# Performance work log

Measured on AMD Instinct MI355X. Metric: run time of the kernel, lower is better.

## Reference

```python
import jax, jax.numpy as jnp
import numpy as np

NREF, NALT, B, D, F = 131072, 32768, 4096, 128, 512
H = F // 2  # d_ffn // 2
EPS = 1e-5


def _ln(x, w, b):
    m = jnp.mean(x, axis=-1, keepdims=True)
    v = jnp.mean((x - m) ** 2, axis=-1, keepdims=True)
    return (x - m) * jax.lax.rsqrt(v + EPS) * w + b


def setup_inputs() -> dict:
    key = jax.random.key(0)
    ks = jax.random.split(key, 16)
    s = 0.02
    return {
        "ref_flat": jax.random.normal(ks[0], (NREF, D), jnp.float32),
        "alt_flat": jax.random.normal(ks[1], (NALT, D), jnp.float32),
        "ref_seg": jnp.sort(jax.random.randint(ks[2], (NREF,), 0, B)),
        "alt_seg": jnp.sort(jax.random.randint(ks[3], (NALT,), 0, B)),
        "norm1_w": jnp.ones((D,), jnp.float32),
        "norm1_b": jnp.zeros((D,), jnp.float32),
        "w1_ref": jax.random.normal(ks[4], (D, F), jnp.float32) * s,
        "b1_ref": jnp.zeros((F,), jnp.float32),
        "w1_alt": jax.random.normal(ks[5], (D, F), jnp.float32) * s,
        "b1_alt": jnp.zeros((F,), jnp.float32),
        "norm2_w": jnp.ones((H,), jnp.float32),
        "norm2_b": jnp.zeros((H,), jnp.float32),
        "alpha_ref": jnp.float32(0.01),
        "alpha_alt": jnp.float32(0.01),
        "beta_ref": jnp.float32(0.01),
        "beta_alt": jnp.float32(0.01),
        "gamma": jnp.float32(0.01),
        "ref_regularizer": 0.1 * jnp.ones((H,), jnp.float32),
        "reg_w_pre": jnp.float32(np.log(0.1)),
        "w2_ref": jax.random.normal(ks[6], (H, D), jnp.float32) * s,
        "b2_ref": jnp.zeros((D,), jnp.float32),
        "w2_alt": jax.random.normal(ks[7], (H, D), jnp.float32) * s,
        "b2_alt": jnp.zeros((D,), jnp.float32),
    }


def reference(ref_flat, alt_flat, ref_seg, alt_seg,
              norm1_w, norm1_b, w1_ref, b1_ref, w1_alt, b1_alt,
              norm2_w, norm2_b, alpha_ref, alpha_alt, beta_ref, beta_alt,
              gamma, ref_regularizer, reg_w_pre, w2_ref, b2_ref, w2_alt, b2_alt):
    # proj1 + SELU on flattened ragged reads
    zr = jax.nn.selu(_ln(ref_flat, norm1_w, norm1_b) @ w1_ref + b1_ref)   # [NREF, F]
    za = jax.nn.selu(_ln(alt_flat, norm1_w, norm1_b) @ w1_alt + b1_alt)   # [NALT, F]
    z1r, z2r = zr[:, :H], zr[:, H:]
    z1a, z2a = za[:, :H], za[:, H:]
    z2r = _ln(z2r, norm2_w, norm2_b)
    z2a = _ln(z2a, norm2_w, norm2_b)

    cnt_r = jax.ops.segment_sum(jnp.ones((NREF,), z2r.dtype), ref_seg, num_segments=B)
    cnt_a = jax.ops.segment_sum(jnp.ones((NALT,), z2a.dtype), alt_seg, num_segments=B)
    reg_w = jnp.exp(reg_w_pre) + 0.25
    # regularized mean field over each ref set
    ref_mf = (jax.ops.segment_sum(z2r, ref_seg, num_segments=B)
              + reg_w * ref_regularizer) / (cnt_r[:, None] + reg_w)       # [B, H]
    alt_mf = jax.ops.segment_sum(z2a, alt_seg, num_segments=B) \
             / jnp.maximum(cnt_a, 1.0)[:, None]                            # [B, H]

    ref_gate = z2r * alpha_ref + 1.0 + (beta_ref * ref_mf)[ref_seg]
    alt_gate = z2a * alpha_alt + 1.0 + (beta_alt * alt_mf + gamma * ref_mf)[alt_seg]

    out_r = ref_flat + (z1r * ref_gate) @ w2_ref + b2_ref
    out_a = alt_flat + (z1a * alt_gate) @ w2_alt + b2_alt
    return out_r, out_a
```

## Files before the change

### kernel.cpp

```cpp
#include <hip/hip_runtime.h>
#include <hip/hip_bf16.h>

#define NREF 131072
#define NALT 32768
#define BSEG 4096
#define D 128
#define F 512
#define H 256
#define EPS 1e-5f

typedef short short8 __attribute__((ext_vector_type(8)));
typedef float f32x4 __attribute__((ext_vector_type(4)));

__device__ __forceinline__ float selu_f(float z) {
    const float sc = 1.0507009873554805f;
    const float al = 1.6732632423543772f;
    return z > 0.f ? sc * z : sc * al * (__expf(z) - 1.f);
}

__device__ __forceinline__ short f2bf(float v) {
    __bf16 b = (__bf16)v;
    return __builtin_bit_cast(short, b);
}

__global__ void pack_w(const float* __restrict__ w, __bf16* __restrict__ wp, int KT, int N) {
    int idx = blockIdx.x * 256 + threadIdx.x;
    int j = idx & 7;
    int l = (idx >> 3) & 63;
    int t = idx >> 9;
    int kt = t % KT;
    int nt = t / KT;
    int k = kt * 32 + ((l >> 4) << 3) + j;
    int n = (nt << 4) + (l & 15);
    wp[idx] = (__bf16)w[k * N + n];
}

__global__ __launch_bounds__(256, 3)
void pass1_kernel(const float* __restrict__ x, const int* __restrict__ seg,
                  const __bf16* __restrict__ w1p, const float* __restrict__ b1,
                  const float* __restrict__ n1w, const float* __restrict__ n1b,
                  const float* __restrict__ n2w, const float* __restrict__ n2b,
                  float* __restrict__ seg_sum, float* __restrict__ seg_cnt) {
    __shared__ __align__(16) __bf16 ys[32 * 128];
    __shared__ float z2s[32][257];
    __shared__ float n2w_s[H], n2b_s[H], b1h_s[H];
    __shared__ int seg_s[32];

    const int tid = threadIdx.x;
    const int lane = tid & 63;
    const int wv = tid >> 6;
    const size_t row0 = (size_t)blockIdx.x * 32;

    short8 bb[4][4];
    #pragma unroll
    for (int p = 0; p < 4; ++p)
        #pragma unroll
        for (int kt = 0; kt < 4; ++kt)
            bb[p][kt] = *reinterpret_cast<const short8*>(
                w1p + ((size_t)((16 + wv * 4 + p) * 4 + kt) * 64 + lane) * 8);

    const int r = tid >> 3, g = tid & 7;
    float xr[16];
    #pragma unroll
    for (int i = 0; i < 4; ++i) {
        float4 t = *reinterpret_cast<const float4*>(x + (row0 + r) * D + g * 16 + i * 4);
        xr[i * 4 + 0] = t.x; xr[i * 4 + 1] = t.y; xr[i * 4 + 2] = t.z; xr[i * 4 + 3] = t.w;
    }
    float w1r[16], c1r[16];
    #pragma unroll
    for (int i = 0; i < 4; ++i) {
        float4 t = *reinterpret_cast<const float4*>(n1w + g * 16 + i * 4);
        w1r[i * 4 + 0] = t.x; w1r[i * 4 + 1] = t.y; w1r[i * 4 + 2] = t.z; w1r[i * 4 + 3] = t.w;
        float4 u = *reinterpret_cast<const float4*>(n1b + g * 16 + i * 4);
        c1r[i * 4 + 0] = u.x; c1r[i * 4 + 1] = u.y; c1r[i * 4 + 2] = u.z; c1r[i * 4 + 3] = u.w;
    }

    n2w_s[tid] = n2w[tid]; n2b_s[tid] = n2b[tid];
    b1h_s[tid] = b1[H + tid];
    if (tid < 32) seg_s[tid] = seg[row0 + tid];

    {
        float s = 0.f, ss = 0.f;
        #pragma unroll
        for (int i = 0; i < 16; ++i) { s += xr[i]; ss += xr[i] * xr[i]; }
        s += __shfl_xor(s, 1); ss += __shfl_xor(ss, 1);
        s += __shfl_xor(s, 2); ss += __shfl_xor(ss, 2);
        s += __shfl_xor(s, 4); ss += __shfl_xor(ss, 4);
        float mean = s * (1.f / 128.f);
        float var = ss * (1.f / 128.f) - mean * mean;
        float rsv = rsqrtf(var + EPS);
        const int swr = (r & 7) << 3;
        #pragma unroll
        for (int h = 0; h < 2; ++h) {
            short8 pk;
            #pragma unroll
            for (int j = 0; j < 8; ++j) {
                pk[j] = f2bf((xr[h * 8 + j] - mean) * rsv * w1r[h * 8 + j] + c1r[h * 8 + j]);
            }
            *reinterpret_cast<short8*>(&ys[r * 128 + ((g * 16 + h * 8) ^ swr)]) = pk;
        }
    }
    __syncthreads();

    {
        const int m0 = lane & 15;
        const int swm = (m0 & 7) << 3;
        const int ccol = (lane >> 4) << 3;
        short8 a0[4], a1[4];
        #pragma unroll
        for (int kt = 0; kt < 4; ++kt) {
            a0[kt] = *reinterpret_cast<const short8*>(&ys[m0 * 128 + ((kt * 32 + ccol) ^ swm)]);
            a1[kt] = *reinterpret_cast<const short8*>(&ys[(m0 + 16) * 128 + ((kt * 32 + ccol) ^ swm)]);
        }
        #pragma unroll
        for (int nt = 0; nt < 4; ++nt) {
            f32x4 acc0 = {0.f, 0.f, 0.f, 0.f};
            f32x4 acc1 = {0.f, 0.f, 0.f, 0.f};
            #pragma unroll
            for (int kt = 0; kt < 4; ++kt) {
                acc0 = __builtin_amdgcn_mfma_f32_16x16x32_bf16(a0[kt], bb[nt][kt], acc0, 0, 0, 0);
                acc1 = __builtin_amdgcn_mfma_f32_16x16x32_bf16(a1[kt], bb[nt][kt], acc1, 0, 0, 0);
            }
            int cz = (wv * 4 + nt) * 16 + m0;
            float bbias = b1h_s[cz];
            #pragma unroll
            for (int reg = 0; reg < 4; ++reg) {
                int r0 = ((lane >> 4) << 2) + reg;
                z2s[r0][cz] = selu_f(acc0[reg] + bbias);
                z2s[r0 + 16][cz] = selu_f(acc1[reg] + bbias);
            }
        }
    }
    __syncthreads();

    {
        float s2 = 0.f, q2 = 0.f;
        float z2c[32];
        #pragma unroll
        for (int c = 0; c < 32; ++c) {
            int col = g * 4 + (c & 3) + ((c >> 2) << 5);
            float v = z2s[r][col];
            z2c[c] = v; s2 += v; q2 += v * v;
        }
        s2 += __shfl_xor(s2, 1); q2 += __shfl_xor(q2, 1);
        s2 += __shfl_xor(s2, 2); q2 += __shfl_xor(q2, 2);
        s2 += __shfl_xor(s2, 4); q2 += __shfl_xor(q2, 4);
        float mean2 = s2 * (1.f / 256.f);
        float var2 = q2 * (1.f / 256.f) - mean2 * mean2;
        float rs2 = rsqrtf(var2 + EPS);
        #pragma unroll
        for (int c = 0; c < 32; ++c) {
            int col = g * 4 + (c & 3) + ((c >> 2) << 5);
            z2s[r][col] = (z2c[c] - mean2) * rs2 * n2w_s[col] + n2b_s[col];
        }
    }
    __syncthreads();

    {
        int c = tid;
        int s_cur = seg_s[0];
        float run = 0.f;
        for (int rr = 0; rr < 32; ++rr) {
            int sg = seg_s[rr];
            if (sg != s_cur) {
                atomicAdd(&seg_sum[(size_t)s_cur * H + c], run);
                run = 0.f; s_cur = sg;
            }
            run += z2s[rr][c];
        }
        atomicAdd(&seg_sum[(size_t)s_cur * H + c], run);
        if (tid == 0) {
            int sc = seg_s[0]; float rl = 0.f;
            for (int rr = 0; rr < 32; ++rr) {
                if (seg_s[rr] != sc) { atomicAdd(&seg_cnt[sc], rl); rl = 0.f; sc = seg_s[rr]; }
                rl += 1.f;
            }
            atomicAdd(&seg_cnt[sc], rl);
        }
    }
}

__global__ void mf_kernel(const float* __restrict__ sum_r, const float* __restrict__ cnt_r,
                          const float* __restrict__ sum_a, const float* __restrict__ cnt_a,
                          const float* __restrict__ regz, const float* __restrict__ reg_w_pre,
                          const float* __restrict__ beta_ref, const float* __restrict__ beta_alt,
                          const float* __restrict__ gamma,
                          float* __restrict__ G_ref, float* __restrict__ G_alt) {
    int s = blockIdx.x, c = threadIdx.x;
    size_t i = (size_t)s * H + c;
    float rw = __expf(reg_w_pre[0]) + 0.25f;
    float mfr = (sum_r[i] + rw * regz[c]) / (cnt_r[s] + rw);
    float mfa = sum_a[i] / fmaxf(cnt_a[s], 1.f);
    G_ref[i] = beta_ref[0] * mfr;
    G_alt[i] = beta_alt[0] * mfa + gamma[0] * mfr;
}

__global__ __launch_bounds__(256, 3)
void pass2_kernel(const float* __restrict__ x, const int* __restrict__ seg,
                  const __bf16* __restrict__ w1p, const float* __restrict__ b1,
                  const __bf16* __restrict__ w2p, const float* __restrict__ b2,
                  const float* __restrict__ n1w, const float* __restrict__ n1b,
                  const float* __restrict__ n2w, const float* __restrict__ n2b,
                  const float* __restrict__ alpha_p, const float* __restrict__ G,
                  float* __restrict__ out) {
    __shared__ __align__(16) __bf16 ys[32 * 128];
    __shared__ __align__(16) __bf16 zs[32 * 512];
    __shared__ float n2w_s[H], n2b_s[H], b1_s[F], b2_s[D];
    __shared__ int seg_s[32];
    __shared__ float alpha_s;

    const int tid = threadIdx.x;
    const int lane = tid & 63;
    const int wv = tid >> 6;
    const size_t row0 = (size_t)blockIdx.x * 32;

    short8 bb[4][4];
    #pragma unroll
    for (int p = 0; p < 4; ++p)
        #pragma unroll
        for (int kt = 0; kt < 4; ++kt)
            bb[p][kt] = *reinterpret_cast<const short8*>(
                w1p + ((size_t)((wv * 8 + p) * 4 + kt) * 64 + lane) * 8);

    const int r = tid >> 3, g = tid & 7;
    float xr[16];
    #pragma unroll
    for (int i = 0; i < 4; ++i) {
        float4 t = *reinterpret_cast<const float4*>(x + (row0 + r) * D + g * 16 + i * 4);
        xr[i * 4 + 0] = t.x; xr[i * 4 + 1] = t.y; xr[i * 4 + 2] = t.z; xr[i * 4 + 3] = t.w;
    }
    float w1r[16], c1r[16];
    #pragma unroll
    for (int i = 0; i < 4; ++i) {
        float4 t = *reinterpret_cast<const float4*>(n1w + g * 16 + i * 4);
        w1r[i * 4 + 0] = t.x; w1r[i * 4 + 1] = t.y; w1r[i * 4 + 2] = t.z; w1r[i * 4 + 3] = t.w;
        float4 u = *reinterpret_cast<const float4*>(n1b + g * 16 + i * 4);
        c1r[i * 4 + 0] = u.x; c1r[i * 4 + 1] = u.y; c1r[i * 4 + 2] = u.z; c1r[i * 4 + 3] = u.w;
    }

    if (tid < D) b2_s[tid] = b2[tid];
    n2w_s[tid] = n2w[tid]; n2b_s[tid] = n2b[tid];
    b1_s[tid] = b1[tid]; b1_s[tid + 256] = b1[tid + 256];
    if (tid < 32) seg_s[tid] = seg[row0 + tid];
    if (tid == 0) alpha_s = alpha_p[0];

    {
        float s = 0.f, ss = 0.f;
        #pragma unroll
        for (int i = 0; i < 16; ++i) { s += xr[i]; ss += xr[i] * xr[i]; }
        s += __shfl_xor(s, 1); ss += __shfl_xor(ss, 1);
        s += __shfl_xor(s, 2); ss += __shfl_xor(ss, 2);
        s += __shfl_xor(s, 4); ss += __shfl_xor(ss, 4);
        float mean = s * (1.f / 128.f);
        float var = ss * (1.f / 128.f) - mean * mean;
        float rsv = rsqrtf(var + EPS);
        const int swr = (r & 7) << 3;
        #pragma unroll
        for (int h = 0; h < 2; ++h) {
            short8 pk;
            #pragma unroll
            for (int j = 0; j < 8; ++j) {
                pk[j] = f2bf((xr[h * 8 + j] - mean) * rsv * w1r[h * 8 + j] + c1r[h * 8 + j]);
            }
            *reinterpret_cast<short8*>(&ys[r * 128 + ((g * 16 + h * 8) ^ swr)]) = pk;
        }
    }
    __syncthreads();

    {
        const int m0 = lane & 15;
        const int swm = (m0 & 7) << 3;
        const int ccol = (lane >> 4) << 3;
        short8 a0[4], a1[4];
        #pragma unroll
        for (int kt = 0; kt < 4; ++kt) {
            a0[kt] = *reinterpret_cast<const short8*>(&ys[m0 * 128 + ((kt * 32 + ccol) ^ swm)]);
            a1[kt] = *reinterpret_cast<const short8*>(&ys[(m0 + 16) * 128 + ((kt * 32 + ccol) ^ swm)]);
        }
        #pragma unroll
        for (int nt = 0; nt < 8; ++nt) {
            f32x4 acc0 = {0.f, 0.f, 0.f, 0.f};
            f32x4 acc1 = {0.f, 0.f, 0.f, 0.f};
            #pragma unroll
            for (int kt = 0; kt < 4; ++kt) {
                acc0 = __builtin_amdgcn_mfma_f32_16x16x32_bf16(a0[kt], bb[nt & 3][kt], acc0, 0, 0, 0);
                acc1 = __builtin_amdgcn_mfma_f32_16x16x32_bf16(a1[kt], bb[nt & 3][kt], acc1, 0, 0, 0);
            }
            if (nt < 4) {
                #pragma unroll
                for (int kt = 0; kt < 4; ++kt)
                    bb[nt & 3][kt] = *reinterpret_cast<const short8*>(
                        w1p + ((size_t)((wv * 8 + nt + 4) * 4 + kt) * 64 + lane) * 8);
            }
            int colg = (wv * 8 + nt) * 16 + m0;
            float bbias = b1_s[colg];
            #pragma unroll
            for (int reg = 0; reg < 4; ++reg) {
                int r0 = ((lane >> 4) << 2) + reg;
                zs[r0 * 512 + (colg ^ ((r0 & 7) << 3))] = (__bf16)selu_f(acc0[reg] + bbias);
                zs[(r0 + 16) * 512 + (colg ^ ((r0 & 7) << 3))] = (__bf16)selu_f(acc1[reg] + bbias);
            }
        }
    }

    short8 b2f[2][8];
    #pragma unroll
    for (int p = 0; p < 2; ++p)
        #pragma unroll
        for (int kt = 0; kt < 8; ++kt)
            b2f[p][kt] = *reinterpret_cast<const short8*>(
                w2p + ((size_t)((wv * 2 + p) * 8 + kt) * 64 + lane) * 8);
    float xres[16];
    #pragma unroll
    for (int p = 0; p < 2; ++p) {
        int col = (wv * 2 + p) * 16 + (lane & 15);
        #pragma unroll
        for (int reg = 0; reg < 4; ++reg) {
            int r0 = ((lane >> 4) << 2) + reg;
            xres[p * 8 + reg]     = x[(row0 + r0) * D + col];
            xres[p * 8 + 4 + reg] = x[(row0 + r0 + 16) * D + col];
        }
    }
    __syncthreads();

    {
        const int swr2 = (r & 7) << 3;
        float s2 = 0.f, q2 = 0.f;
        float z2c[32];
        #pragma unroll
        for (int c = 0; c < 32; ++c) {
            int col = g * 4 + (c & 3) + ((c >> 2) << 5);
            float v = (float)zs[r * 512 + ((256 + col) ^ swr2)];
            z2c[c] = v; s2 += v; q2 += v * v;
        }
        s2 += __shfl_xor(s2, 1); q2 += __shfl_xor(q2, 1);
        s2 += __shfl_xor(s2, 2); q2 += __shfl_xor(q2, 2);
        s2 += __shfl_xor(s2, 4); q2 += __shfl_xor(q2, 4);
        float mean2 = s2 * (1.f / 256.f);
        float var2 = q2 * (1.f / 256.f) - mean2 * mean2;
        float rs2 = rsqrtf(var2 + EPS);
        const float* Grow = G + (size_t)seg_s[r] * H;
        float al = alpha_s;
        #pragma unroll
        for (int c = 0; c < 32; ++c) {
            int col = g * 4 + (c & 3) + ((c >> 2) << 5);
            float z2n = (z2c[c] - mean2) * rs2 * n2w_s[col] + n2b_s[col];
            float gate = z2n * al + 1.f + Grow[col];
            int idx = r * 512 + (col ^ swr2);
            zs[idx] = (__bf16)((float)zs[idx] * gate);
        }
    }
    __syncthreads();

    {
        const int m0 = lane & 15;
        const int swm = (m0 & 7) << 3;
        const int ccol = (lane >> 4) << 3;
        f32x4 zero = {0.f, 0.f, 0.f, 0.f};
        f32x4 acc[2][2] = {{zero, zero}, {zero, zero}};
        #pragma unroll
        for (int kt = 0; kt < 8; ++kt) {
            short8 a0 = *reinterpret_cast<const short8*>(&zs[m0 * 512 + ((kt * 32 + ccol) ^ swm)]);
            short8 a1 = *reinterpret_cast<const short8*>(&zs[(m0 + 16) * 512 + ((kt * 32 + ccol) ^ swm)]);
            #pragma unroll
            for (int p = 0; p < 2; ++p) {
                acc[p][0] = __builtin_amdgcn_mfma_f32_16x16x32_bf16(a0, b2f[p][kt], acc[p][0], 0, 0, 0);
                acc[p][1] = __builtin_amdgcn_mfma_f32_16x16x32_bf16(a1, b2f[p][kt], acc[p][1], 0, 0, 0);
            }
        }
        #pragma unroll
        for (int p = 0; p < 2; ++p) {
            int col = (wv * 2 + p) * 16 + m0;
            float b2v = b2_s[col];
            #pragma unroll
            for (int reg = 0; reg < 4; ++reg) {
                int r0 = ((lane >> 4) << 2) + reg;
                out[(row0 + r0) * D + col]      = acc[p][0][reg] + b2v + xres[p * 8 + reg];
                out[(row0 + r0 + 16) * D + col] = acc[p][1][reg] + b2v + xres[p * 8 + 4 + reg];
            }
        }
    }
}

extern "C" void kernel_launch(void* const* d_in, const int* in_sizes, int n_in,
                              void* d_out, int out_size, void* d_ws, size_t ws_size,
                              hipStream_t stream) {
    const float* ref_flat = (const float*)d_in[0];
    const float* alt_flat = (const float*)d_in[1];
    const int*   ref_seg  = (const int*)d_in[2];
    const int*   alt_seg  = (const int*)d_in[3];
    const float* norm1_w  = (const float*)d_in[4];
    const float* norm1_b  = (const float*)d_in[5];
    const float* w1_ref   = (const float*)d_in[6];
    const float* b1_ref   = (const float*)d_in[7];
    const float* w1_alt   = (const float*)d_in[8];
    const float* b1_alt   = (const float*)d_in[9];
    const float* norm2_w  = (const float*)d_in[10];
    const float* norm2_b  = (const float*)d_in[11];
    const float* alpha_ref = (const float*)d_in[12];
    const float* alpha_alt = (const float*)d_in[13];
    const float* beta_ref  = (const float*)d_in[14];
    const float* beta_alt  = (const float*)d_in[15];
    const float* gamma     = (const float*)d_in[16];
    const float* ref_regularizer = (const float*)d_in[17];
    const float* reg_w_pre = (const float*)d_in[18];
    const float* w2_ref   = (const float*)d_in[19];
    const float* b2_ref   = (const float*)d_in[20];
    const float* w2_alt   = (const float*)d_in[21];
    const float* b2_alt   = (const float*)d_in[22];

    char* ws = (char*)d_ws;
    float* sum_r = (float*)(ws);
    float* sum_a = (float*)(ws + 4194304);
    float* cnt_r = (float*)(ws + 8388608);
    float* cnt_a = (float*)(ws + 8404992);
    float* G_ref = (float*)(ws + 8421376);
    float* G_alt = (float*)(ws + 12615680);
    __bf16* w1p_r = (__bf16*)(ws + 16809984);
    __bf16* w1p_a = (__bf16*)(ws + 16941056);
    __bf16* w2p_r = (__bf16*)(ws + 17072128);
    __bf16* w2p_a = (__bf16*)(ws + 17137664);

    hipMemsetAsync(d_ws, 0, 8421376, stream);

    pack_w<<<256, 256, 0, stream>>>(w1_ref, w1p_r, 4, F);
    pack_w<<<256, 256, 0, stream>>>(w1_alt, w1p_a, 4, F);
    pack_w<<<128, 256, 0, stream>>>(w2_ref, w2p_r, 8, D);
    pack_w<<<128, 256, 0, stream>>>(w2_alt, w2p_a, 8, D);

    pass1_kernel<<<NREF/32, 256, 0, stream>>>(ref_flat, ref_seg, w1p_r, b1_ref,
                                              norm1_w, norm1_b, norm2_w, norm2_b, sum_r, cnt_r);
    pass1_kernel<<<NALT/32, 256, 0, stream>>>(alt_flat, alt_seg, w1p_a, b1_alt,
                                              norm1_w, norm1_b, norm2_w, norm2_b, sum_a, cnt_a);

    mf_kernel<<<BSEG, 256, 0, stream>>>(sum_r, cnt_r, sum_a, cnt_a, ref_regularizer, reg_w_pre,
                                        beta_ref, beta_alt, gamma, G_ref, G_alt);

    pass2_kernel<<<NREF/32, 256, 0, stream>>>(ref_flat, ref_seg, w1p_r, b1_ref, w2p_r, b2_ref,
                                              norm1_w, norm1_b, norm2_w, norm2_b,
                                              alpha_ref, G_ref, (float*)d_out);
    pass2_kernel<<<NALT/32, 256, 0, stream>>>(alt_flat, alt_seg, w1p_a, b1_alt, w2p_a, b2_alt,
                                              norm1_w, norm1_b, norm2_w, norm2_b,
                                              alpha_alt, G_alt, (float*)d_out + (size_t)NREF * D);
}
```

Baseline: 370.2 us.

## Cache normalized z2 from pass1 and skip recomputing its GEMM half in pass2

Pass1 now writes the layer-normed z2 half as bf16 to a workspace buffer. Pass2 reads it back instead of recomputing the second half of the first projection and its layernorm, which halves pass2's first GEMM and shrinks its shared memory. The launch order is changed to ref pass1 → mf_ref → ref pass2 → alt pass1 → mf_alt → alt pass2 so the one buffer can be reused. Occupancy hints rise to 4 and z2 staging moves to bf16 LDS. In exchange it adds a 64 MB bf16 write and read per ref pass and stores z2 at lower precision before the segment sums.

```diff
diff --git a/kernel.cpp b/kernel.cpp
--- a/kernel.cpp
+++ b/kernel.cpp
@@ -21,6 +21,10 @@
 __device__ __forceinline__ short f2bf(float v) {
     __bf16 b = (__bf16)v;
     return __builtin_bit_cast(short, b);
+}
+
+__device__ __forceinline__ float bf2f(short s) {
+    return (float)__builtin_bit_cast(__bf16, s);
 }
 
 __global__ void pack_w(const float* __restrict__ w, __bf16* __restrict__ wp, int KT, int N) {
@@ -35,29 +39,34 @@
     wp[idx] = (__bf16)w[k * N + n];
 }
 
-__global__ __launch_bounds__(256, 3)
+__global__ __launch_bounds__(256, 4)
 void pass1_kernel(const float* __restrict__ x, const int* __restrict__ seg,
                   const __bf16* __restrict__ w1p, const float* __restrict__ b1,
                   const float* __restrict__ n1w, const float* __restrict__ n1b,
                   const float* __restrict__ n2w, const float* __restrict__ n2b,
-                  float* __restrict__ seg_sum, float* __restrict__ seg_cnt) {
+                  float* __restrict__ seg_sum, float* __restrict__ seg_cnt,
+                  __bf16* __restrict__ z2n_out) {
     __shared__ __align__(16) __bf16 ys[32 * 128];
-    __shared__ float z2s[32][257];
-    __shared__ float n2w_s[H], n2b_s[H], b1h_s[H];
+    __shared__ __align__(16) __bf16 z2s[32 * 256];
+    __shared__ float n2w_s[H], n2b_s[H];
     __shared__ int seg_s[32];
 
     const int tid = threadIdx.x;
     const int lane = tid & 63;
     const int wv = tid >> 6;
+    const int q = lane >> 4, m0 = lane & 15;
     const size_t row0 = (size_t)blockIdx.x * 32;
 
-    short8 bb[4][4];
-    #pragma unroll
-    for (int p = 0; p < 4; ++p)
+    short8 bb[2][4];
+    #pragma unroll
+    for (int p = 0; p < 2; ++p)
         #pragma unroll
         for (int kt = 0; kt < 4; ++kt)
             bb[p][kt] = *reinterpret_cast<const short8*>(
                 w1p + ((size_t)((16 + wv * 4 + p) * 4 + kt) * 64 + lane) * 8);
+    float b1v[4];
+    #pragma unroll
+    for (int nt = 0; nt < 4; ++nt) b1v[nt] = b1[256 + (wv * 4 + nt) * 16 + m0];
 
     const int r = tid >> 3, g = tid & 7;
     float xr[16];
@@ -76,7 +85,6 @@
     }
 
     n2w_s[tid] = n2w[tid]; n2b_s[tid] = n2b[tid];
-    b1h_s[tid] = b1[H + tid];
     if (tid < 32) seg_s[tid] = seg[row0 + tid];
 
     {
@@ -94,18 +102,16 @@
         for (int h = 0; h < 2; ++h) {
             short8 pk;
             #pragma unroll
-            for (int j = 0; j < 8; ++j) {
+            for (int j = 0; j < 8; ++j)
                 pk[j] = f2bf((xr[h * 8 + j] - mean) * rsv * w1r[h * 8 + j] + c1r[h * 8 + j]);
-            }
             *reinterpret_cast<short8*>(&ys[r * 128 + ((g * 16 + h * 8) ^ swr)]) = pk;
         }
     }
     __syncthreads();
 
     {
-        const int m0 = lane & 15;
         const int swm = (m0 & 7) << 3;
-        const int ccol = (lane >> 4) << 3;
+        const int ccol = q << 3;
         short8 a0[4], a1[4];
         #pragma unroll
         for (int kt = 0; kt < 4; ++kt) {
@@ -118,29 +124,39 @@
             f32x4 acc1 = {0.f, 0.f, 0.f, 0.f};
             #pragma unroll
             for (int kt = 0; kt < 4; ++kt) {
-                acc0 = __builtin_amdgcn_mfma_f32_16x16x32_bf16(a0[kt], bb[nt][kt], acc0, 0, 0, 0);
-                acc1 = __builtin_amdgcn_mfma_f32_16x16x32_bf16(a1[kt], bb[nt][kt], acc1, 0, 0, 0);
+                acc0 = __builtin_amdgcn_mfma_f32_16x16x32_bf16(a0[kt], bb[nt & 1][kt], acc0, 0, 0, 0);
+                acc1 = __builtin_amdgcn_mfma_f32_16x16x32_bf16(a1[kt], bb[nt & 1][kt], acc1, 0, 0, 0);
+            }
+            if (nt < 2) {
+                #pragma unroll
+                for (int kt = 0; kt < 4; ++kt)
+                    bb[nt & 1][kt] = *reinterpret_cast<const short8*>(
+                        w1p + ((size_t)((16 + wv * 4 + nt + 2) * 4 + kt) * 64 + lane) * 8);
             }
             int cz = (wv * 4 + nt) * 16 + m0;
-            float bbias = b1h_s[cz];
             #pragma unroll
             for (int reg = 0; reg < 4; ++reg) {
-                int r0 = ((lane >> 4) << 2) + reg;
-                z2s[r0][cz] = selu_f(acc0[reg] + bbias);
-                z2s[r0 + 16][cz] = selu_f(acc1[reg] + bbias);
-            }
-        }
-    }
-    __syncthreads();
-
-    {
+                int r0 = (q << 2) + reg;
+                int r1 = r0 + 16;
+                z2s[r0 * 256 + (cz ^ ((r0 & 7) << 3))] = (__bf16)selu_f(acc0[reg] + b1v[nt]);
+                z2s[r1 * 256 + (cz ^ ((r1 & 7) << 3))] = (__bf16)selu_f(acc1[reg] + b1v[nt]);
+            }
+        }
+    }
+    __syncthreads();
+
+    {
+        const int swr = (r & 7) << 3;
+        float vb[32];
         float s2 = 0.f, q2 = 0.f;
-        float z2c[32];
-        #pragma unroll
-        for (int c = 0; c < 32; ++c) {
-            int col = g * 4 + (c & 3) + ((c >> 2) << 5);
-            float v = z2s[r][col];
-            z2c[c] = v; s2 += v; q2 += v * v;
+        #pragma unroll
+        for (int i = 0; i < 4; ++i) {
+            short8 v = *reinterpret_cast<const short8*>(&z2s[r * 256 + ((g * 32 + i * 8) ^ swr)]);
+            #pragma unroll
+            for (int j = 0; j < 8; ++j) {
+                float f = bf2f(v[j]);
+                vb[i * 8 + j] = f; s2 += f; q2 += f * f;
+            }
         }
         s2 += __shfl_xor(s2, 1); q2 += __shfl_xor(q2, 1);
         s2 += __shfl_xor(s2, 2); q2 += __shfl_xor(q2, 2);
@@ -149,9 +165,15 @@
         float var2 = q2 * (1.f / 256.f) - mean2 * mean2;
         float rs2 = rsqrtf(var2 + EPS);
         #pragma unroll
-        for (int c = 0; c < 32; ++c) {
-            int col = g * 4 + (c & 3) + ((c >> 2) << 5);
-            z2s[r][col] = (z2c[c] - mean2) * rs2 * n2w_s[col] + n2b_s[col];
+        for (int i = 0; i < 4; ++i) {
+            short8 o;
+            #pragma unroll
+            for (int j = 0; j < 8; ++j) {
+                int col = g * 32 + i * 8 + j;
+                o[j] = f2bf((vb[i * 8 + j] - mean2) * rs2 * n2w_s[col] + n2b_s[col]);
+            }
+            *reinterpret_cast<short8*>(&z2s[r * 256 + ((g * 32 + i * 8) ^ swr)]) = o;
+            *reinterpret_cast<short8*>(z2n_out + (row0 + r) * H + g * 32 + i * 8) = o;
         }
     }
     __syncthreads();
@@ -166,7 +188,7 @@
                 atomicAdd(&seg_sum[(size_t)s_cur * H + c], run);
                 run = 0.f; s_cur = sg;
             }
-            run += z2s[rr][c];
+            run += (float)z2s[rr * 256 + (c ^ ((rr & 7) << 3))];
         }
         atomicAdd(&seg_sum[(size_t)s_cur * H + c], run);
         if (tid == 0) {
@@ -180,49 +202,60 @@
     }
 }
 
-__global__ void mf_kernel(const float* __restrict__ sum_r, const float* __restrict__ cnt_r,
-                          const float* __restrict__ sum_a, const float* __restrict__ cnt_a,
-                          const float* __restrict__ regz, const float* __restrict__ reg_w_pre,
-                          const float* __restrict__ beta_ref, const float* __restrict__ beta_alt,
-                          const float* __restrict__ gamma,
-                          float* __restrict__ G_ref, float* __restrict__ G_alt) {
+__global__ void mf_ref_kernel(const float* __restrict__ sum_r, const float* __restrict__ cnt_r,
+                              const float* __restrict__ regz, const float* __restrict__ reg_w_pre,
+                              const float* __restrict__ beta_ref, float* __restrict__ G_ref) {
+    int s = blockIdx.x, c = threadIdx.x;
+    size_t i = (size_t)s * H + c;
+    float rw = __expf(reg_w_pre[0]) + 0.25f;
+    float mfr = (sum_r[i] + rw * regz[c]) / (cnt_r[s] + rw);
+    G_ref[i] = beta_ref[0] * mfr;
+}
+
+__global__ void mf_alt_kernel(const float* __restrict__ sum_r, const float* __restrict__ cnt_r,
+                              const float* __restrict__ sum_a, const float* __restrict__ cnt_a,
+                              const float* __restrict__ regz, const float* __restrict__ reg_w_pre,
+                              const float* __restrict__ beta_alt, const float* __restrict__ gamma,
+                              float* __restrict__ G_alt) {
     int s = blockIdx.x, c = threadIdx.x;
     size_t i = (size_t)s * H + c;
     float rw = __expf(reg_w_pre[0]) + 0.25f;
     float mfr = (sum_r[i] + rw * regz[c]) / (cnt_r[s] + rw);
     float mfa = sum_a[i] / fmaxf(cnt_a[s], 1.f);
-    G_ref[i] = beta_ref[0] * mfr;
     G_alt[i] = beta_alt[0] * mfa + gamma[0] * mfr;
 }
 
-__global__ __launch_bounds__(256, 3)
+__global__ __launch_bounds__(256, 4)
 void pass2_kernel(const float* __restrict__ x, const int* __restrict__ seg,
                   const __bf16* __restrict__ w1p, const float* __restrict__ b1,
                   const __bf16* __restrict__ w2p, const float* __restrict__ b2,
                   const float* __restrict__ n1w, const float* __restrict__ n1b,
-                  const float* __restrict__ n2w, const float* __restrict__ n2b,
                   const float* __restrict__ alpha_p, const float* __restrict__ G,
-                  float* __restrict__ out) {
+                  const __bf16* __restrict__ z2n, float* __restrict__ out) {
     __shared__ __align__(16) __bf16 ys[32 * 128];
-    __shared__ __align__(16) __bf16 zs[32 * 512];
-    __shared__ float n2w_s[H], n2b_s[H], b1_s[F], b2_s[D];
-    __shared__ int seg_s[32];
-    __shared__ float alpha_s;
+    __shared__ __align__(16) __bf16 zs[32 * 256];
 
     const int tid = threadIdx.x;
     const int lane = tid & 63;
     const int wv = tid >> 6;
+    const int q = lane >> 4, m0 = lane & 15;
     const size_t row0 = (size_t)blockIdx.x * 32;
-
-    short8 bb[4][4];
-    #pragma unroll
-    for (int p = 0; p < 4; ++p)
+    const int r = tid >> 3, g = tid & 7;
+
+    short8 bb[2][4];
+    #pragma unroll
+    for (int p = 0; p < 2; ++p)
         #pragma unroll
         for (int kt = 0; kt < 4; ++kt)
             bb[p][kt] = *reinterpret_cast<const short8*>(
-                w1p + ((size_t)((wv * 8 + p) * 4 + kt) * 64 + lane) * 8);
-
-    const int r = tid >> 3, g = tid & 7;
+                w1p + ((size_t)((wv * 4 + p) * 4 + kt) * 64 + lane) * 8);
+    float b1v[4];
+    #pragma unroll
+    for (int nt = 0; nt < 4; ++nt) b1v[nt] = b1[(wv * 4 + nt) * 16 + m0];
+
+    const int segi = seg[row0 + r];
+    const float alpha = alpha_p[0];
+
     float xr[16];
     #pragma unroll
     for (int i = 0; i < 4; ++i) {
@@ -237,12 +270,6 @@
         float4 u = *reinterpret_cast<const float4*>(n1b + g * 16 + i * 4);
         c1r[i * 4 + 0] = u.x; c1r[i * 4 + 1] = u.y; c1r[i * 4 + 2] = u.z; c1r[i * 4 + 3] = u.w;
     }
-
-    if (tid < D) b2_s[tid] = b2[tid];
-    n2w_s[tid] = n2w[tid]; n2b_s[tid] = n2b[tid];
-    b1_s[tid] = b1[tid]; b1_s[tid + 256] = b1[tid + 256];
-    if (tid < 32) seg_s[tid] = seg[row0 + tid];
-    if (tid == 0) alpha_s = alpha_p[0];
 
     {
         float s = 0.f, ss = 0.f;
@@ -259,18 +286,16 @@
         for (int h = 0; h < 2; ++h) {
             short8 pk;
             #pragma unroll
-            for (int j = 0; j < 8; ++j) {
+            for (int j = 0; j < 8; ++j)
                 pk[j] = f2bf((xr[h * 8 + j] - mean) * rsv * w1r[h * 8 + j] + c1r[h * 8 + j]);
-            }
             *reinterpret_cast<short8*>(&ys[r * 128 + ((g * 16 + h * 8) ^ swr)]) = pk;
         }
     }
     __syncthreads();
 
     {
-        const int m0 = lane & 15;
         const int swm = (m0 & 7) << 3;
-        const int ccol = (lane >> 4) << 3;
+        const int ccol = q << 3;
         short8 a0[4], a1[4];
         #pragma unroll
         for (int kt = 0; kt < 4; ++kt) {
@@ -278,31 +303,44 @@
             a1[kt] = *reinterpret_cast<const short8*>(&ys[(m0 + 16) * 128 + ((kt * 32 + ccol) ^ swm)]);
         }
         #pragma unroll
-        for (int nt = 0; nt < 8; ++nt) {
+        for (int nt = 0; nt < 4; ++nt) {
             f32x4 acc0 = {0.f, 0.f, 0.f, 0.f};
             f32x4 acc1 = {0.f, 0.f, 0.f, 0.f};
             #pragma unroll
             for (int kt = 0; kt < 4; ++kt) {
-                acc0 = __builtin_amdgcn_mfma_f32_16x16x32_bf16(a0[kt], bb[nt & 3][kt], acc0, 0, 0, 0);
-                acc1 = __builtin_amdgcn_mfma_f32_16x16x32_bf16(a1[kt], bb[nt & 3][kt], acc1, 0, 0, 0);
-            }
-            if (nt < 4) {
+                acc0 = __builtin_amdgcn_mfma_f32_16x16x32_bf16(a0[kt], bb[nt & 1][kt], acc0, 0, 0, 0);
+                acc1 = __builtin_amdgcn_mfma_f32_16x16x32_bf16(a1[kt], bb[nt & 1][kt], acc1, 0, 0, 0);
+            }
+            if (nt < 2) {
                 #pragma unroll
                 for (int kt = 0; kt < 4; ++kt)
-                    bb[nt & 3][kt] = *reinterpret_cast<const short8*>(
-                        w1p + ((size_t)((wv * 8 + nt + 4) * 4 + kt) * 64 + lane) * 8);
-            }
-            int colg = (wv * 8 + nt) * 16 + m0;
-            float bbias = b1_s[colg];
+                    bb[nt & 1][kt] = *reinterpret_cast<const short8*>(
+                        w1p + ((size_t)((wv * 4 + nt + 2) * 4 + kt) * 64 + lane) * 8);
+            }
+            int cz = (wv * 4 + nt) * 16 + m0;
             #pragma unroll
             for (int reg = 0; reg < 4; ++reg) {
-                int r0 = ((lane >> 4) << 2) + reg;
-                zs[r0 * 512 + (colg ^ ((r0 & 7) << 3))] = (__bf16)selu_f(acc0[reg] + bbias);
-                zs[(r0 + 16) * 512 + (colg ^ ((r0 & 7) << 3))] = (__bf16)selu_f(acc1[reg] + bbias);
-            }
-        }
-    }
-
+                int r0 = (q << 2) + reg;
+                int r1 = r0 + 16;
+                zs[r0 * 256 + (cz ^ ((r0 & 7) << 3))] = (__bf16)selu_f(acc0[reg] + b1v[nt]);
+                zs[r1 * 256 + (cz ^ ((r1 & 7) << 3))] = (__bf16)selu_f(acc1[reg] + b1v[nt]);
+            }
+        }
+    }
+
+    short8 zn[4];
+    #pragma unroll
+    for (int i = 0; i < 4; ++i)
+        zn[i] = *reinterpret_cast<const short8*>(z2n + (row0 + r) * H + g * 32 + i * 8);
+    float gvf[32];
+    {
+        const float* Gp = G + (size_t)segi * H + g * 32;
+        #pragma unroll
+        for (int i = 0; i < 8; ++i) {
+            float4 t = *reinterpret_cast<const float4*>(Gp + i * 4);
+            gvf[i * 4 + 0] = t.x; gvf[i * 4 + 1] = t.y; gvf[i * 4 + 2] = t.z; gvf[i * 4 + 3] = t.w;
+        }
+    }
     short8 b2f[2][8];
     #pragma unroll
     for (int p = 0; p < 2; ++p)
@@ -310,13 +348,33 @@
         for (int kt = 0; kt < 8; ++kt)
             b2f[p][kt] = *reinterpret_cast<const short8*>(
                 w2p + ((size_t)((wv * 2 + p) * 8 + kt) * 64 + lane) * 8);
+    float b2v[2];
+    #pragma unroll
+    for (int p = 0; p < 2; ++p) b2v[p] = b2[(wv * 2 + p) * 16 + m0];
+    __syncthreads();
+
+    {
+        const int swr = (r & 7) << 3;
+        #pragma unroll
+        for (int i = 0; i < 4; ++i) {
+            int idx = r * 256 + ((g * 32 + i * 8) ^ swr);
+            short8 v = *reinterpret_cast<const short8*>(&zs[idx]);
+            short8 o;
+            #pragma unroll
+            for (int j = 0; j < 8; ++j) {
+                float gate = bf2f(zn[i][j]) * alpha + 1.f + gvf[i * 8 + j];
+                o[j] = f2bf(bf2f(v[j]) * gate);
+            }
+            *reinterpret_cast<short8*>(&zs[idx]) = o;
+        }
+    }
     float xres[16];
     #pragma unroll
     for (int p = 0; p < 2; ++p) {
-        int col = (wv * 2 + p) * 16 + (lane & 15);
+        int col = (wv * 2 + p) * 16 + m0;
         #pragma unroll
         for (int reg = 0; reg < 4; ++reg) {
-            int r0 = ((lane >> 4) << 2) + reg;
+            int r0 = (q << 2) + reg;
             xres[p * 8 + reg]     = x[(row0 + r0) * D + col];
             xres[p * 8 + 4 + reg] = x[(row0 + r0 + 16) * D + col];
         }
@@ -324,44 +382,14 @@
     __syncthreads();
 
     {
-        const int swr2 = (r & 7) << 3;
-        float s2 = 0.f, q2 = 0.f;
-        float z2c[32];
-        #pragma unroll
-        for (int c = 0; c < 32; ++c) {
-            int col = g * 4 + (c & 3) + ((c >> 2) << 5);
-            float v = (float)zs[r * 512 + ((256 + col) ^ swr2)];
-            z2c[c] = v; s2 += v; q2 += v * v;
-        }
-        s2 += __shfl_xor(s2, 1); q2 += __shfl_xor(q2, 1);
-        s2 += __shfl_xor(s2, 2); q2 += __shfl_xor(q2, 2);
-        s2 += __shfl_xor(s2, 4); q2 += __shfl_xor(q2, 4);
-        float mean2 = s2 * (1.f / 256.f);
-        float var2 = q2 * (1.f / 256.f) - mean2 * mean2;
-        float rs2 = rsqrtf(var2 + EPS);
-        const float* Grow = G + (size_t)seg_s[r] * H;
-        float al = alpha_s;
-        #pragma unroll
-        for (int c = 0; c < 32; ++c) {
-            int col = g * 4 + (c & 3) + ((c >> 2) << 5);
-            float z2n = (z2c[c] - mean2) * rs2 * n2w_s[col] + n2b_s[col];
-            float gate = z2n * al + 1.f + Grow[col];
-            int idx = r * 512 + (col ^ swr2);
-            zs[idx] = (__bf16)((float)zs[idx] * gate);
-        }
-    }
-    __syncthreads();
-
-    {
-        const int m0 = lane & 15;
         const int swm = (m0 & 7) << 3;
-        const int ccol = (lane >> 4) << 3;
+        const int ccol = q << 3;
         f32x4 zero = {0.f, 0.f, 0.f, 0.f};
         f32x4 acc[2][2] = {{zero, zero}, {zero, zero}};
         #pragma unroll
         for (int kt = 0; kt < 8; ++kt) {
-            short8 a0 = *reinterpret_cast<const short8*>(&zs[m0 * 512 + ((kt * 32 + ccol) ^ swm)]);
-            short8 a1 = *reinterpret_cast<const short8*>(&zs[(m0 + 16) * 512 + ((kt * 32 + ccol) ^ swm)]);
+            short8 a0 = *reinterpret_cast<const short8*>(&zs[m0 * 256 + ((kt * 32 + ccol) ^ swm)]);
+            short8 a1 = *reinterpret_cast<const short8*>(&zs[(m0 + 16) * 256 + ((kt * 32 + ccol) ^ swm)]);
             #pragma unroll
             for (int p = 0; p < 2; ++p) {
                 acc[p][0] = __builtin_amdgcn_mfma_f32_16x16x32_bf16(a0, b2f[p][kt], acc[p][0], 0, 0, 0);
@@ -371,12 +399,11 @@
         #pragma unroll
         for (int p = 0; p < 2; ++p) {
             int col = (wv * 2 + p) * 16 + m0;
-            float b2v = b2_s[col];
             #pragma unroll
             for (int reg = 0; reg < 4; ++reg) {
-                int r0 = ((lane >> 4) << 2) + reg;
-                out[(row0 + r0) * D + col]      = acc[p][0][reg] + b2v + xres[p * 8 + reg];
-                out[(row0 + r0 + 16) * D + col] = acc[p][1][reg] + b2v + xres[p * 8 + 4 + reg];
+                int r0 = (q << 2) + reg;
+                out[(row0 + r0) * D + col]      = acc[p][0][reg] + b2v[p] + xres[p * 8 + reg];
+                out[(row0 + r0 + 16) * D + col] = acc[p][1][reg] + b2v[p] + xres[p * 8 + 4 + reg];
             }
         }
     }
@@ -420,6 +447,7 @@
     __bf16* w1p_a = (__bf16*)(ws + 16941056);
     __bf16* w2p_r = (__bf16*)(ws + 17072128);
     __bf16* w2p_a = (__bf16*)(ws + 17137664);
+    __bf16* z2nb  = (__bf16*)(ws + 17203200);
 
     hipMemsetAsync(d_ws, 0, 8421376, stream);
 
@@ -429,17 +457,21 @@
     pack_w<<<128, 256, 0, stream>>>(w2_alt, w2p_a, 8, D);
 
     pass1_kernel<<<NREF/32, 256, 0, stream>>>(ref_flat, ref_seg, w1p_r, b1_ref,
-                                              norm1_w, norm1_b, norm2_w, norm2_b, sum_r, cnt_r);
+                                              norm1_w, norm1_b, norm2_w, norm2_b,
+                                              sum_r, cnt_r, z2nb);
+    mf_ref_kernel<<<BSEG, 256, 0, stream>>>(sum_r, cnt_r, ref_regularizer, reg_w_pre,
+                                            beta_ref, G_ref);
+    pass2_kernel<<<NREF/32, 256, 0, stream>>>(ref_flat, ref_seg, w1p_r, b1_ref, w2p_r, b2_ref,
+                                              norm1_w, norm1_b, alpha_ref, G_ref, z2nb,
+                                              (float*)d_out);
+
     pass1_kernel<<<NALT/32, 256, 0, stream>>>(alt_flat, alt_seg, w1p_a, b1_alt,
-                                              norm1_w, norm1_b, norm2_w, norm2_b, sum_a, cnt_a);
-
-    mf_kernel<<<BSEG, 256, 0, stream>>>(sum_r, cnt_r, sum_a, cnt_a, ref_regularizer, reg_w_pre,
-                                        beta_ref, beta_alt, gamma, G_ref, G_alt);
-
-    pass2_kernel<<<NREF/32, 256, 0, stream>>>(ref_flat, ref_seg, w1p_r, b1_ref, w2p_r, b2_ref,
                                               norm1_w, norm1_b, norm2_w, norm2_b,
-                                              alpha_ref, G_ref, (float*)d_out);
+                                              sum_a, cnt_a, z2nb);
+    mf_alt_kernel<<<BSEG, 256, 0, stream>>>(sum_r, cnt_r, sum_a, cnt_a,
+                                            ref_regularizer, reg_w_pre,
+                                            beta_alt, gamma, G_alt);
     pass2_kernel<<<NALT/32, 256, 0, stream>>>(alt_flat, alt_seg, w1p_a, b1_alt, w2p_a, b2_alt,
-                                              norm1_w, norm1_b, norm2_w, norm2_b,
-                                              alpha_alt, G_alt, (float*)d_out + (size_t)NREF * D);
-}
+                                              norm1_w, norm1_b, alpha_alt, G_alt, z2nb,
+                                              (float*)d_out + (size_t)NREF * D);
+}
```

Measured after the change: 324.3 us. 12.4% less time.
